# Performance work log

Measured on AMD Instinct MI355X. Metric: run time of the kernel, lower is better.

The kernel has to match this reference:

```python
import jax, jax.numpy as jnp
import numpy as np

N = 50000      # n_nodes
E = 800000     # n_edges (before self-loops)
IN = 256       # in_channels
MID = 512      # mid_channel
MID2 = MID // 2
OUT = 64       # out_channels


def setup_inputs() -> dict:
    key = jax.random.key(0)
    ks = jax.random.split(key, 16)
    def w(k, shape):
        fan_in = shape[0]
        return jax.random.normal(k, shape, jnp.float32) * (1.0 / np.sqrt(fan_in))
    return {
        "node_feature": jax.random.normal(ks[0], (N, IN), jnp.float32),
        "edge_index": jax.random.randint(ks[1], (2, E), 0, N, jnp.int32),
        # GCNConv weights (PyG convention: x @ W, bias added after aggregation)
        "Wg1": w(ks[2], (IN, MID)),   "bg1": jnp.zeros((MID,), jnp.float32),
        "Wg2": w(ks[3], (MID, MID2)), "bg2": jnp.zeros((MID2,), jnp.float32),
        "Wg3": w(ks[4], (MID2, OUT)), "bg3": jnp.zeros((OUT,), jnp.float32),
        # parallel Linear layers
        "Wl1": w(ks[5], (IN, MID)),   "bl1": jnp.zeros((MID,), jnp.float32),
        "Wl2": w(ks[6], (MID, MID2)), "bl2": jnp.zeros((MID2,), jnp.float32),
        "Wl3": w(ks[7], (MID2, OUT)), "bl3": jnp.zeros((OUT,), jnp.float32),
    }


def reference(node_feature, edge_index, Wg1, bg1, Wg2, bg2, Wg3, bg3,
              Wl1, bl1, Wl2, bl2, Wl3, bl3):
    n = node_feature.shape[0]
    # list_add_self_loops: append (i, i) for every node
    loops = jnp.arange(n, dtype=edge_index.dtype)
    src = jnp.concatenate([edge_index[0], loops])
    dst = jnp.concatenate([edge_index[1], loops])
    # symmetric GCN normalization: deg computed on graph with self-loops
    deg = jax.ops.segment_sum(jnp.ones_like(dst, jnp.float32), dst, num_segments=n)
    dis = jax.lax.rsqrt(jnp.maximum(deg, 1.0))  # deg >= 1 thanks to self-loops
    norm = dis[src] * dis[dst]                  # [E'] edge coefficients

    def gcn_conv(x, W, b):
        h = x @ W                                            # [N, F_out]
        msgs = h[src] * norm[:, None]                        # gather + scale
        return jax.ops.segment_sum(msgs, dst, num_segments=n) + b  # scatter-add

    h1 = jax.nn.elu(gcn_conv(node_feature, Wg1, bg1)) + node_feature @ Wl1 + bl1
    h2 = jax.nn.elu(gcn_conv(h1, Wg2, bg2)) + h1 @ Wl2 + bl2
    out = gcn_conv(h2, Wg3, bg3) + h2 @ Wl3 + bl3
    return out
```

## Files before the change

### kernel.cpp

```cpp
#include <hip/hip_runtime.h>
#include <hip/hip_bf16.h>
#include <math.h>

#define IN_CH  256
#define MID    512
#define MID2   256
#define OUT_CH 64

typedef __attribute__((ext_vector_type(8))) short s16x8;
typedef __attribute__((ext_vector_type(4))) float f32x4;


__global__ __launch_bounds__(256) void deg_kernel(const int* __restrict__ dst,
                                                  int* __restrict__ cnt, int E) {
  int stride = gridDim.x * blockDim.x;
  for (int e = blockIdx.x * blockDim.x + threadIdx.x; e < E; e += stride)
    atomicAdd(&cnt[dst[e]], 1);
}

__global__ __launch_bounds__(1024) void scan_dis_kernel(const int* __restrict__ cnt,
                                                        int* __restrict__ rowstart,
                                                        float* __restrict__ dis, int N) {
  __shared__ int part[1024];
  int t = threadIdx.x;
  int chunk = (N + 1023) >> 10;
  int lo = t * chunk;
  int hi = lo + chunk; if (hi > N) hi = N; if (lo > N) lo = N;
  int s = 0;
  for (int i = lo; i < hi; ++i) s += cnt[i] + 1;
  part[t] = s;
  __syncthreads();
  for (int off = 1; off < 1024; off <<= 1) {
    int v = (t >= off) ? part[t - off] : 0;
    __syncthreads();
    part[t] += v;
    __syncthreads();
  }
  int base = part[t] - s;
  for (int i = lo; i < hi; ++i) {
    int d = cnt[i] + 1;
    rowstart[i] = base;
    dis[i] = rsqrtf((float)d);
    base += d;
  }
  if (t == 1023) rowstart[N] = part[1023];
}

__global__ __launch_bounds__(256) void fill_adj_kernel(const int* __restrict__ src,
                                                       const int* __restrict__ dst,
                                                       const int* __restrict__ rowstart,
                                                       int* __restrict__ cnt2,
                                                       int* __restrict__ adj,
                                                       int E, int N) {
  int total = E + N;
  int stride = gridDim.x * blockDim.x;
  for (int e = blockIdx.x * blockDim.x + threadIdx.x; e < total; e += stride) {
    int s, d;
    if (e < E) { s = src[e]; d = dst[e]; }
    else       { s = d = e - E; }
    int pos = rowstart[d] + atomicAdd(&cnt2[d], 1);
    adj[pos] = s;
  }
}


__device__ inline unsigned bf16_rne(float v) {
  unsigned u = __float_as_uint(v);
  return (u + 0x7FFFu + ((u >> 16) & 1u)) >> 16;
}

__global__ __launch_bounds__(256) void wsplit_kernel(const float* __restrict__ W,
                                                     short* __restrict__ Wt_hi,
                                                     short* __restrict__ Wt_lo,
                                                     int K, int Fout) {
  int idx = blockIdx.x * 256 + threadIdx.x;
  if (idx >= K * Fout) return;
  int k = idx / Fout, n = idx - k * Fout;
  float v = W[idx];
  unsigned h = bf16_rne(v);
  float hf = __uint_as_float(h << 16);
  unsigned l = bf16_rne(v - hf);
  Wt_hi[(size_t)n * K + k] = (short)h;
  Wt_lo[(size_t)n * K + k] = (short)l;
}


template<bool ADD_BIAS>
__global__ __launch_bounds__(256, 2)
void gemm_mfma3(const float* __restrict__ A, const short* __restrict__ Bth,
                const short* __restrict__ Btl, const float* __restrict__ bias,
                float* __restrict__ C, int Nrows, int K, int Fout) {
  __shared__ short lds[4 * 128 * 64];
  short* Ah = lds;
  short* Al = lds + 8192;
  short* Bh = lds + 16384;
  short* Bl = lds + 24576;

  const int tid  = threadIdx.x;
  const int lane = tid & 63;
  const int wid  = tid >> 6;
  const int wr = wid >> 1, wc = wid & 1;
  const int row0 = blockIdx.x * 128;
  const int col0 = blockIdx.y * 128;

  f32x4 acc[4][4] = {};

  const int sr    = tid >> 1;
  const int shalf = (tid & 1) << 5;
  int arow = row0 + sr; if (arow > Nrows - 1) arow = Nrows - 1;
  const float* Abase  = A   + (size_t)arow * K + shalf;
  const short* Bhbase = Bth + (size_t)(col0 + sr) * K + shalf;
  const short* Blbase = Btl + (size_t)(col0 + sr) * K + shalf;
  int wslot[4];
  #pragma unroll
  for (int i = 0; i < 4; ++i)
    wslot[i] = sr * 64 + ((((shalf >> 3) + i) ^ (sr & 7)) << 3);

  for (int k0 = 0; k0 < K; k0 += 64) {
    float4 av[8];
    const float* ap = Abase + k0;
    #pragma unroll
    for (int i = 0; i < 8; ++i) av[i] = *(const float4*)(ap + i * 4);
    s16x8 rbh[4], rbl[4];
    const short* bp = Bhbase + k0;
    const short* bq = Blbase + k0;
    #pragma unroll
    for (int i = 0; i < 4; ++i) rbh[i] = *(const s16x8*)(bp + i * 8);
    #pragma unroll
    for (int i = 0; i < 4; ++i) rbl[i] = *(const s16x8*)(bq + i * 8);

    __syncthreads();

    #pragma unroll
    for (int i = 0; i < 4; ++i) {
      s16x8 hi, lo;
      #pragma unroll
      for (int j = 0; j < 2; ++j) {
        float4 v = av[i * 2 + j];
        float vv[4] = {v.x, v.y, v.z, v.w};
        #pragma unroll
        for (int m = 0; m < 4; ++m) {
          unsigned h = bf16_rne(vv[m]);
          float hf = __uint_as_float(h << 16);
          unsigned l = bf16_rne(vv[m] - hf);
          hi[j * 4 + m] = (short)h;
          lo[j * 4 + m] = (short)l;
        }
      }
      *(s16x8*)(Ah + wslot[i]) = hi;
      *(s16x8*)(Al + wslot[i]) = lo;
    }
    #pragma unroll
    for (int i = 0; i < 4; ++i) {
      *(s16x8*)(Bh + wslot[i]) = rbh[i];
      *(s16x8*)(Bl + wslot[i]) = rbl[i];
    }
    __syncthreads();

    #pragma unroll
    for (int ks = 0; ks < 2; ++ks) {
      const int sw = ((((ks << 2) + (lane >> 4)) ^ (lane & 7)) << 3);
      s16x8 fah[4], fal[4], fbh[4], fbl[4];
      #pragma unroll
      for (int mi = 0; mi < 4; ++mi) {
        int base = (wr * 64 + mi * 16 + (lane & 15)) * 64 + sw;
        fah[mi] = *(const s16x8*)(Ah + base);
        fal[mi] = *(const s16x8*)(Al + base);
      }
      #pragma unroll
      for (int ni = 0; ni < 4; ++ni) {
        int base = (wc * 64 + ni * 16 + (lane & 15)) * 64 + sw;
        fbh[ni] = *(const s16x8*)(Bh + base);
        fbl[ni] = *(const s16x8*)(Bl + base);
      }
      #pragma unroll
      for (int mi = 0; mi < 4; ++mi)
        #pragma unroll
        for (int ni = 0; ni < 4; ++ni) {
          acc[mi][ni] = __builtin_amdgcn_mfma_f32_16x16x32_bf16(fah[mi], fbh[ni], acc[mi][ni], 0, 0, 0);
          acc[mi][ni] = __builtin_amdgcn_mfma_f32_16x16x32_bf16(fah[mi], fbl[ni], acc[mi][ni], 0, 0, 0);
          acc[mi][ni] = __builtin_amdgcn_mfma_f32_16x16x32_bf16(fal[mi], fbh[ni], acc[mi][ni], 0, 0, 0);
        }
    }
  }

  #pragma unroll
  for (int mi = 0; mi < 4; ++mi) {
    #pragma unroll
    for (int r = 0; r < 4; ++r) {
      int rr = row0 + wr * 64 + mi * 16 + (lane >> 4) * 4 + r;
      if (rr >= Nrows) continue;
      #pragma unroll
      for (int ni = 0; ni < 4; ++ni) {
        int cc = col0 + wc * 64 + ni * 16 + (lane & 15);
        float v = acc[mi][ni][r];
        if (ADD_BIAS) v += bias[cc];
        C[(size_t)rr * Fout + cc] = v;
      }
    }
  }
}


template<bool ADD_BIAS>
__global__ __launch_bounds__(256) void gemm64(const float* __restrict__ A,
                                              const float* __restrict__ W,
                                              const float* __restrict__ bias,
                                              float* __restrict__ C,
                                              int Nrows, int K, int Fout) {
  __shared__ float As[16][64];
  __shared__ float Bs[16][64];
  const int tid  = threadIdx.x;
  const int row0 = blockIdx.x * 64;
  const int col0 = blockIdx.y * 64;
  const int tx   = tid & 15;
  const int ty   = tid >> 4;
  const int la_r = tid >> 2;
  const int la_c = (tid & 3) << 2;
  const int lb_r = tid >> 4;
  const int lb_c = (tid & 15) << 2;

  float acc[4][4];
  #pragma unroll
  for (int i = 0; i < 4; ++i)
    #pragma unroll
    for (int j = 0; j < 4; ++j) acc[i][j] = 0.f;

  for (int k0 = 0; k0 < K; k0 += 16) {
    float4 av = make_float4(0.f, 0.f, 0.f, 0.f);
    int ar = row0 + la_r;
    if (ar < Nrows) av = *(const float4*)(A + (size_t)ar * K + (k0 + la_c));
    float4 bv = *(const float4*)(W + (size_t)(k0 + lb_r) * Fout + (col0 + lb_c));
    __syncthreads();
    As[la_c + 0][la_r] = av.x;
    As[la_c + 1][la_r] = av.y;
    As[la_c + 2][la_r] = av.z;
    As[la_c + 3][la_r] = av.w;
    *(float4*)&Bs[lb_r][lb_c] = bv;
    __syncthreads();
    #pragma unroll
    for (int k = 0; k < 16; ++k) {
      float4 a4 = *(const float4*)&As[k][ty << 2];
      float4 b4 = *(const float4*)&Bs[k][tx << 2];
      float a[4] = {a4.x, a4.y, a4.z, a4.w};
      float b[4] = {b4.x, b4.y, b4.z, b4.w};
      #pragma unroll
      for (int i = 0; i < 4; ++i)
        #pragma unroll
        for (int j = 0; j < 4; ++j) acc[i][j] = fmaf(a[i], b[j], acc[i][j]);
    }
  }

  #pragma unroll
  for (int i = 0; i < 4; ++i) {
    int r = row0 + (ty << 2) + i;
    if (r < Nrows) {
      float4 v = make_float4(acc[i][0], acc[i][1], acc[i][2], acc[i][3]);
      if (ADD_BIAS) {
        const float* bp = bias + col0 + (tx << 2);
        v.x += bp[0]; v.y += bp[1]; v.z += bp[2]; v.w += bp[3];
      }
      *(float4*)(C + (size_t)r * Fout + col0 + (tx << 2)) = v;
    }
  }
}


__device__ inline void fma4(float4& a, const float4 q, const float w) {
  a.x = fmaf(q.x, w, a.x); a.y = fmaf(q.y, w, a.y);
  a.z = fmaf(q.z, w, a.z); a.w = fmaf(q.w, w, a.w);
}

template<int F, bool DO_ELU>
__global__ __launch_bounds__(256) void agg_kernel(const float* __restrict__ H,
                                                  const int* __restrict__ adj,
                                                  const int* __restrict__ rowstart,
                                                  const float* __restrict__ dis,
                                                  const float* __restrict__ bias,
                                                  float* __restrict__ out, int N) {
  constexpr int VF = F / 64;
  constexpr int NV = (VF >= 4) ? VF / 4 : 1;
  int node = (int)((blockIdx.x * blockDim.x + threadIdx.x) >> 6);
  int lane = threadIdx.x & 63;
  if (node >= N) return;
  int e = rowstart[node];
  const int end = rowstart[node + 1];

  if constexpr (VF >= 4) {
    float4 acc[NV] = {};
    const char* base = (const char*)H + (size_t)lane * (VF * 4);
    const size_t rstride = (size_t)F * 4;
    for (; e + 4 <= end; e += 4) {
      int s0 = adj[e], s1 = adj[e + 1], s2 = adj[e + 2], s3 = adj[e + 3];
      float w0 = dis[s0], w1 = dis[s1], w2 = dis[s2], w3 = dis[s3];
      const float4* p0 = (const float4*)(base + s0 * rstride);
      const float4* p1 = (const float4*)(base + s1 * rstride);
      const float4* p2 = (const float4*)(base + s2 * rstride);
      const float4* p3 = (const float4*)(base + s3 * rstride);
      #pragma unroll
      for (int v = 0; v < NV; ++v) {
        float4 q0 = p0[v], q1 = p1[v], q2 = p2[v], q3 = p3[v];
        fma4(acc[v], q0, w0); fma4(acc[v], q1, w1);
        fma4(acc[v], q2, w2); fma4(acc[v], q3, w3);
      }
    }
    for (; e < end; ++e) {
      int s = adj[e]; float w = dis[s];
      const float4* p = (const float4*)(base + s * rstride);
      #pragma unroll
      for (int v = 0; v < NV; ++v) fma4(acc[v], p[v], w);
    }
    float di = dis[node];
    float* op = out + (size_t)node * F + lane * VF;
    const float* bp = bias + lane * VF;
    #pragma unroll
    for (int v = 0; v < NV; ++v) {
      float vals[4] = {acc[v].x, acc[v].y, acc[v].z, acc[v].w};
      #pragma unroll
      for (int j = 0; j < 4; ++j) {
        float val = fmaf(vals[j], di, bp[v * 4 + j]);
        if (DO_ELU) val = (val > 0.f) ? val : expm1f(val);
        op[v * 4 + j] += val;
      }
    }
  } else {
    float acc = 0.f;
    for (; e + 4 <= end; e += 4) {
      int s0 = adj[e], s1 = adj[e + 1], s2 = adj[e + 2], s3 = adj[e + 3];
      float w0 = dis[s0], w1 = dis[s1], w2 = dis[s2], w3 = dis[s3];
      float q0 = H[(size_t)s0 * F + lane], q1 = H[(size_t)s1 * F + lane];
      float q2 = H[(size_t)s2 * F + lane], q3 = H[(size_t)s3 * F + lane];
      acc = fmaf(q0, w0, acc); acc = fmaf(q1, w1, acc);
      acc = fmaf(q2, w2, acc); acc = fmaf(q3, w3, acc);
    }
    for (; e < end; ++e) {
      int s = adj[e];
      acc = fmaf(H[(size_t)s * F + lane], dis[s], acc);
    }
    float val = fmaf(acc, dis[node], bias[lane]);
    if (DO_ELU) val = (val > 0.f) ? val : expm1f(val);
    out[(size_t)node * F + lane] += val;
  }
}


static inline char* ws_align(char*& ws, size_t bytes) {
  ws = (char*)(((uintptr_t)ws + 63) & ~(uintptr_t)63);
  char* p = ws;
  ws += bytes;
  return p;
}

extern "C" void kernel_launch(void* const* d_in, const int* in_sizes, int n_in,
                              void* d_out, int out_size, void* d_ws, size_t ws_size,
                              hipStream_t stream) {
  const float* x   = (const float*)d_in[0];
  const int*  eidx = (const int*)d_in[1];
  const float* Wg1 = (const float*)d_in[2];
  const float* bg1 = (const float*)d_in[3];
  const float* Wg2 = (const float*)d_in[4];
  const float* bg2 = (const float*)d_in[5];
  const float* Wg3 = (const float*)d_in[6];
  const float* bg3 = (const float*)d_in[7];
  const float* Wl1 = (const float*)d_in[8];
  const float* bl1 = (const float*)d_in[9];
  const float* Wl2 = (const float*)d_in[10];
  const float* bl2 = (const float*)d_in[11];
  const float* Wl3 = (const float*)d_in[12];
  const float* bl3 = (const float*)d_in[13];

  const int N = in_sizes[0] / IN_CH;
  const int E = in_sizes[1] / 2;
  const int* esrc = eidx;
  const int* edst = eidx + E;

  char* ws = (char*)d_ws;
  float* h1       = (float*)ws_align(ws, (size_t)N * MID  * 4);
  float* h2       = (float*)ws_align(ws, (size_t)N * MID2 * 4);
  float* Hb       = (float*)ws_align(ws, (size_t)N * MID  * 4);
  float* dis      = (float*)ws_align(ws, (size_t)N * 4);
  int*   rowstart = (int*)ws_align(ws, (size_t)(N + 1) * 4);
  int*   cnt      = (int*)ws_align(ws, (size_t)N * 4);
  int*   cnt2     = (int*)ws_align(ws, (size_t)N * 4);
  int*   adj      = (int*)ws_align(ws, (size_t)(E + N) * 4);
  short* wl1h = (short*)ws_align(ws, (size_t)IN_CH * MID  * 2);
  short* wl1l = (short*)ws_align(ws, (size_t)IN_CH * MID  * 2);
  short* wg1h = (short*)ws_align(ws, (size_t)IN_CH * MID  * 2);
  short* wg1l = (short*)ws_align(ws, (size_t)IN_CH * MID  * 2);
  short* wl2h = (short*)ws_align(ws, (size_t)MID * MID2 * 2);
  short* wl2l = (short*)ws_align(ws, (size_t)MID * MID2 * 2);
  short* wg2h = (short*)ws_align(ws, (size_t)MID * MID2 * 2);
  short* wg2l = (short*)ws_align(ws, (size_t)MID * MID2 * 2);

  hipMemsetAsync(cnt, 0, (size_t)2 * N * 4, stream);
  hipMemsetAsync(cnt2, 0, (size_t)N * 4, stream);
  deg_kernel<<<1024, 256, 0, stream>>>(edst, cnt, E);
  scan_dis_kernel<<<1, 1024, 0, stream>>>(cnt, rowstart, dis, N);
  fill_adj_kernel<<<2048, 256, 0, stream>>>(esrc, edst, rowstart, cnt2, adj, E, N);

  {
    int n1 = IN_CH * MID, n2 = MID * MID2;
    wsplit_kernel<<<(n1 + 255) / 256, 256, 0, stream>>>(Wl1, wl1h, wl1l, IN_CH, MID);
    wsplit_kernel<<<(n1 + 255) / 256, 256, 0, stream>>>(Wg1, wg1h, wg1l, IN_CH, MID);
    wsplit_kernel<<<(n2 + 255) / 256, 256, 0, stream>>>(Wl2, wl2h, wl2l, MID, MID2);
    wsplit_kernel<<<(n2 + 255) / 256, 256, 0, stream>>>(Wg2, wg2h, wg2l, MID, MID2);
  }

  int aggBlocks = (N + 3) / 4;
  int rowBlocks = (N + 127) / 128;

  dim3 g1(rowBlocks, MID / 128);
  gemm_mfma3<true ><<<g1, 256, 0, stream>>>(x, wl1h, wl1l, bl1, h1, N, IN_CH, MID);
  gemm_mfma3<false><<<g1, 256, 0, stream>>>(x, wg1h, wg1l, nullptr, Hb, N, IN_CH, MID);
  agg_kernel<MID, true><<<aggBlocks, 256, 0, stream>>>(Hb, adj, rowstart, dis, bg1, h1, N);

  dim3 g2(rowBlocks, MID2 / 128);
  gemm_mfma3<true ><<<g2, 256, 0, stream>>>(h1, wl2h, wl2l, bl2, h2, N, MID, MID2);
  gemm_mfma3<false><<<g2, 256, 0, stream>>>(h1, wg2h, wg2l, nullptr, Hb, N, MID, MID2);
  agg_kernel<MID2, true><<<aggBlocks, 256, 0, stream>>>(Hb, adj, rowstart, dis, bg2, h2, N);

  float* outp = (float*)d_out;
  dim3 g3((N + 63) / 64, OUT_CH / 64);
  gemm64<true ><<<g3, 256, 0, stream>>>(h2, Wl3, bl3, outp, N, MID2, OUT_CH);
  gemm64<false><<<g3, 256, 0, stream>>>(h2, Wg3, nullptr, Hb, N, MID2, OUT_CH);
  agg_kernel<OUT_CH, false><<<aggBlocks, 256, 0, stream>>>(Hb, adj, rowstart, dis, bg3, outp, N);
}
```

Before: 1.062 ms.

## Fuse linear and GCN GEMMs per layer, store GCN features in bf16

```diff
diff --git a/kernel.cpp b/kernel.cpp
--- a/kernel.cpp
+++ b/kernel.cpp
@@ -69,27 +69,28 @@
   return (u + 0x7FFFu + ((u >> 16) & 1u)) >> 16;
 }
 
-__global__ __launch_bounds__(256) void wsplit_kernel(const float* __restrict__ W,
-                                                     short* __restrict__ Wt_hi,
-                                                     short* __restrict__ Wt_lo,
-                                                     int K, int Fout) {
+__global__ __launch_bounds__(256) void wsplit_cat(const float* __restrict__ W,
+                                                  short* __restrict__ Th,
+                                                  short* __restrict__ Tl,
+                                                  int K, int F, int noff) {
   int idx = blockIdx.x * 256 + threadIdx.x;
-  if (idx >= K * Fout) return;
-  int k = idx / Fout, n = idx - k * Fout;
+  if (idx >= K * F) return;
+  int k = idx / F, n = idx - k * F;
   float v = W[idx];
   unsigned h = bf16_rne(v);
   float hf = __uint_as_float(h << 16);
   unsigned l = bf16_rne(v - hf);
-  Wt_hi[(size_t)n * K + k] = (short)h;
-  Wt_lo[(size_t)n * K + k] = (short)l;
-}
-
-
-template<bool ADD_BIAS>
+  Th[(size_t)(noff + n) * K + k] = (short)h;
+  Tl[(size_t)(noff + n) * K + k] = (short)l;
+}
+
+
+template<bool OUT2_BF16>
 __global__ __launch_bounds__(256, 2)
-void gemm_mfma3(const float* __restrict__ A, const short* __restrict__ Bth,
-                const short* __restrict__ Btl, const float* __restrict__ bias,
-                float* __restrict__ C, int Nrows, int K, int Fout) {
+void gemm_dual(const float* __restrict__ A, const short* __restrict__ Bth,
+               const short* __restrict__ Btl, const float* __restrict__ bias1,
+               float* __restrict__ C1, void* __restrict__ C2,
+               int Nrows, int K, int F1) {
   __shared__ short lds[4 * 128 * 64];
   short* Ah = lds;
   short* Al = lds + 8192;
@@ -194,153 +195,101 @@
       for (int ni = 0; ni < 4; ++ni) {
         int cc = col0 + wc * 64 + ni * 16 + (lane & 15);
         float v = acc[mi][ni][r];
-        if (ADD_BIAS) v += bias[cc];
-        C[(size_t)rr * Fout + cc] = v;
+        if (cc < F1) {
+          C1[(size_t)rr * F1 + cc] = v + bias1[cc];
+        } else {
+          int c2 = cc - F1;
+          if (OUT2_BF16)
+            ((unsigned short*)C2)[(size_t)rr * F1 + c2] = (unsigned short)bf16_rne(v);
+          else
+            ((float*)C2)[(size_t)rr * F1 + c2] = v;
+        }
       }
     }
   }
 }
 
 
-template<bool ADD_BIAS>
-__global__ __launch_bounds__(256) void gemm64(const float* __restrict__ A,
-                                              const float* __restrict__ W,
-                                              const float* __restrict__ bias,
-                                              float* __restrict__ C,
-                                              int Nrows, int K, int Fout) {
-  __shared__ float As[16][64];
-  __shared__ float Bs[16][64];
-  const int tid  = threadIdx.x;
-  const int row0 = blockIdx.x * 64;
-  const int col0 = blockIdx.y * 64;
-  const int tx   = tid & 15;
-  const int ty   = tid >> 4;
-  const int la_r = tid >> 2;
-  const int la_c = (tid & 3) << 2;
-  const int lb_r = tid >> 4;
-  const int lb_c = (tid & 15) << 2;
-
-  float acc[4][4];
-  #pragma unroll
-  for (int i = 0; i < 4; ++i)
-    #pragma unroll
-    for (int j = 0; j < 4; ++j) acc[i][j] = 0.f;
-
-  for (int k0 = 0; k0 < K; k0 += 16) {
-    float4 av = make_float4(0.f, 0.f, 0.f, 0.f);
-    int ar = row0 + la_r;
-    if (ar < Nrows) av = *(const float4*)(A + (size_t)ar * K + (k0 + la_c));
-    float4 bv = *(const float4*)(W + (size_t)(k0 + lb_r) * Fout + (col0 + lb_c));
-    __syncthreads();
-    As[la_c + 0][la_r] = av.x;
-    As[la_c + 1][la_r] = av.y;
-    As[la_c + 2][la_r] = av.z;
-    As[la_c + 3][la_r] = av.w;
-    *(float4*)&Bs[lb_r][lb_c] = bv;
-    __syncthreads();
-    #pragma unroll
-    for (int k = 0; k < 16; ++k) {
-      float4 a4 = *(const float4*)&As[k][ty << 2];
-      float4 b4 = *(const float4*)&Bs[k][tx << 2];
-      float a[4] = {a4.x, a4.y, a4.z, a4.w};
-      float b[4] = {b4.x, b4.y, b4.z, b4.w};
-      #pragma unroll
-      for (int i = 0; i < 4; ++i)
-        #pragma unroll
-        for (int j = 0; j < 4; ++j) acc[i][j] = fmaf(a[i], b[j], acc[i][j]);
-    }
-  }
-
-  #pragma unroll
-  for (int i = 0; i < 4; ++i) {
-    int r = row0 + (ty << 2) + i;
-    if (r < Nrows) {
-      float4 v = make_float4(acc[i][0], acc[i][1], acc[i][2], acc[i][3]);
-      if (ADD_BIAS) {
-        const float* bp = bias + col0 + (tx << 2);
-        v.x += bp[0]; v.y += bp[1]; v.z += bp[2]; v.w += bp[3];
-      }
-      *(float4*)(C + (size_t)r * Fout + col0 + (tx << 2)) = v;
-    }
-  }
-}
-
-
-__device__ inline void fma4(float4& a, const float4 q, const float w) {
-  a.x = fmaf(q.x, w, a.x); a.y = fmaf(q.y, w, a.y);
-  a.z = fmaf(q.z, w, a.z); a.w = fmaf(q.w, w, a.w);
-}
-
 template<int F, bool DO_ELU>
-__global__ __launch_bounds__(256) void agg_kernel(const float* __restrict__ H,
-                                                  const int* __restrict__ adj,
-                                                  const int* __restrict__ rowstart,
-                                                  const float* __restrict__ dis,
-                                                  const float* __restrict__ bias,
-                                                  float* __restrict__ out, int N) {
+__global__ __launch_bounds__(256) void agg_bf16(const unsigned short* __restrict__ H,
+                                                const int* __restrict__ adj,
+                                                const int* __restrict__ rowstart,
+                                                const float* __restrict__ dis,
+                                                const float* __restrict__ bias,
+                                                float* __restrict__ out, int N) {
   constexpr int VF = F / 64;
-  constexpr int NV = (VF >= 4) ? VF / 4 : 1;
+  typedef __attribute__((ext_vector_type(VF))) unsigned short uvec;
   int node = (int)((blockIdx.x * blockDim.x + threadIdx.x) >> 6);
   int lane = threadIdx.x & 63;
   if (node >= N) return;
   int e = rowstart[node];
   const int end = rowstart[node + 1];
 
-  if constexpr (VF >= 4) {
-    float4 acc[NV] = {};
-    const char* base = (const char*)H + (size_t)lane * (VF * 4);
-    const size_t rstride = (size_t)F * 4;
-    for (; e + 4 <= end; e += 4) {
-      int s0 = adj[e], s1 = adj[e + 1], s2 = adj[e + 2], s3 = adj[e + 3];
-      float w0 = dis[s0], w1 = dis[s1], w2 = dis[s2], w3 = dis[s3];
-      const float4* p0 = (const float4*)(base + s0 * rstride);
-      const float4* p1 = (const float4*)(base + s1 * rstride);
-      const float4* p2 = (const float4*)(base + s2 * rstride);
-      const float4* p3 = (const float4*)(base + s3 * rstride);
-      #pragma unroll
-      for (int v = 0; v < NV; ++v) {
-        float4 q0 = p0[v], q1 = p1[v], q2 = p2[v], q3 = p3[v];
-        fma4(acc[v], q0, w0); fma4(acc[v], q1, w1);
-        fma4(acc[v], q2, w2); fma4(acc[v], q3, w3);
-      }
-    }
-    for (; e < end; ++e) {
-      int s = adj[e]; float w = dis[s];
-      const float4* p = (const float4*)(base + s * rstride);
-      #pragma unroll
-      for (int v = 0; v < NV; ++v) fma4(acc[v], p[v], w);
-    }
-    float di = dis[node];
-    float* op = out + (size_t)node * F + lane * VF;
-    const float* bp = bias + lane * VF;
-    #pragma unroll
-    for (int v = 0; v < NV; ++v) {
-      float vals[4] = {acc[v].x, acc[v].y, acc[v].z, acc[v].w};
-      #pragma unroll
-      for (int j = 0; j < 4; ++j) {
-        float val = fmaf(vals[j], di, bp[v * 4 + j]);
-        if (DO_ELU) val = (val > 0.f) ? val : expm1f(val);
-        op[v * 4 + j] += val;
-      }
-    }
-  } else {
-    float acc = 0.f;
-    for (; e + 4 <= end; e += 4) {
-      int s0 = adj[e], s1 = adj[e + 1], s2 = adj[e + 2], s3 = adj[e + 3];
-      float w0 = dis[s0], w1 = dis[s1], w2 = dis[s2], w3 = dis[s3];
-      float q0 = H[(size_t)s0 * F + lane], q1 = H[(size_t)s1 * F + lane];
-      float q2 = H[(size_t)s2 * F + lane], q3 = H[(size_t)s3 * F + lane];
-      acc = fmaf(q0, w0, acc); acc = fmaf(q1, w1, acc);
-      acc = fmaf(q2, w2, acc); acc = fmaf(q3, w3, acc);
-    }
-    for (; e < end; ++e) {
-      int s = adj[e];
-      acc = fmaf(H[(size_t)s * F + lane], dis[s], acc);
-    }
-    float val = fmaf(acc, dis[node], bias[lane]);
+  float acc[VF] = {};
+  const unsigned short* base = H + (size_t)lane * VF;
+  for (; e + 4 <= end; e += 4) {
+    int s0 = adj[e], s1 = adj[e + 1], s2 = adj[e + 2], s3 = adj[e + 3];
+    float w0 = dis[s0], w1 = dis[s1], w2 = dis[s2], w3 = dis[s3];
+    uvec v0 = *(const uvec*)(base + (size_t)s0 * F);
+    uvec v1 = *(const uvec*)(base + (size_t)s1 * F);
+    uvec v2 = *(const uvec*)(base + (size_t)s2 * F);
+    uvec v3 = *(const uvec*)(base + (size_t)s3 * F);
+    #pragma unroll
+    for (int j = 0; j < VF; ++j) {
+      acc[j] = fmaf(__uint_as_float((unsigned)v0[j] << 16), w0, acc[j]);
+      acc[j] = fmaf(__uint_as_float((unsigned)v1[j] << 16), w1, acc[j]);
+      acc[j] = fmaf(__uint_as_float((unsigned)v2[j] << 16), w2, acc[j]);
+      acc[j] = fmaf(__uint_as_float((unsigned)v3[j] << 16), w3, acc[j]);
+    }
+  }
+  for (; e < end; ++e) {
+    int s = adj[e]; float w = dis[s];
+    uvec v = *(const uvec*)(base + (size_t)s * F);
+    #pragma unroll
+    for (int j = 0; j < VF; ++j)
+      acc[j] = fmaf(__uint_as_float((unsigned)v[j] << 16), w, acc[j]);
+  }
+
+  float di = dis[node];
+  float* op = out + (size_t)node * F + lane * VF;
+  const float* bp = bias + lane * VF;
+  #pragma unroll
+  for (int j = 0; j < VF; ++j) {
+    float val = fmaf(acc[j], di, bp[j]);
     if (DO_ELU) val = (val > 0.f) ? val : expm1f(val);
-    out[(size_t)node * F + lane] += val;
-  }
+    op[j] += val;
+  }
+}
+
+
+template<int F, bool DO_ELU>
+__global__ __launch_bounds__(256) void agg_f32(const float* __restrict__ H,
+                                               const int* __restrict__ adj,
+                                               const int* __restrict__ rowstart,
+                                               const float* __restrict__ dis,
+                                               const float* __restrict__ bias,
+                                               float* __restrict__ out, int N) {
+  int node = (int)((blockIdx.x * blockDim.x + threadIdx.x) >> 6);
+  int lane = threadIdx.x & 63;
+  if (node >= N) return;
+  int e = rowstart[node];
+  const int end = rowstart[node + 1];
+  float acc = 0.f;
+  for (; e + 4 <= end; e += 4) {
+    int s0 = adj[e], s1 = adj[e + 1], s2 = adj[e + 2], s3 = adj[e + 3];
+    float w0 = dis[s0], w1 = dis[s1], w2 = dis[s2], w3 = dis[s3];
+    float q0 = H[(size_t)s0 * F + lane], q1 = H[(size_t)s1 * F + lane];
+    float q2 = H[(size_t)s2 * F + lane], q3 = H[(size_t)s3 * F + lane];
+    acc = fmaf(q0, w0, acc); acc = fmaf(q1, w1, acc);
+    acc = fmaf(q2, w2, acc); acc = fmaf(q3, w3, acc);
+  }
+  for (; e < end; ++e) {
+    int s = adj[e];
+    acc = fmaf(H[(size_t)s * F + lane], dis[s], acc);
+  }
+  float val = fmaf(acc, dis[node], bias[lane]);
+  if (DO_ELU) val = (val > 0.f) ? val : expm1f(val);
+  out[(size_t)node * F + lane] += val;
 }
 
 
@@ -375,53 +324,51 @@
   const int* edst = eidx + E;
 
   char* ws = (char*)d_ws;
-  float* h1       = (float*)ws_align(ws, (size_t)N * MID  * 4);
-  float* h2       = (float*)ws_align(ws, (size_t)N * MID2 * 4);
-  float* Hb       = (float*)ws_align(ws, (size_t)N * MID  * 4);
+  float* h1   = (float*)ws_align(ws, (size_t)N * MID  * 4);
+  float* h2   = (float*)ws_align(ws, (size_t)N * MID2 * 4);
+  unsigned short* Hbf = (unsigned short*)ws_align(ws, (size_t)N * MID * 2);
+  float* Hb3  = (float*)ws_align(ws, (size_t)N * OUT_CH * 4);
   float* dis      = (float*)ws_align(ws, (size_t)N * 4);
   int*   rowstart = (int*)ws_align(ws, (size_t)(N + 1) * 4);
   int*   cnt      = (int*)ws_align(ws, (size_t)N * 4);
   int*   cnt2     = (int*)ws_align(ws, (size_t)N * 4);
   int*   adj      = (int*)ws_align(ws, (size_t)(E + N) * 4);
-  short* wl1h = (short*)ws_align(ws, (size_t)IN_CH * MID  * 2);
-  short* wl1l = (short*)ws_align(ws, (size_t)IN_CH * MID  * 2);
-  short* wg1h = (short*)ws_align(ws, (size_t)IN_CH * MID  * 2);
-  short* wg1l = (short*)ws_align(ws, (size_t)IN_CH * MID  * 2);
-  short* wl2h = (short*)ws_align(ws, (size_t)MID * MID2 * 2);
-  short* wl2l = (short*)ws_align(ws, (size_t)MID * MID2 * 2);
-  short* wg2h = (short*)ws_align(ws, (size_t)MID * MID2 * 2);
-  short* wg2l = (short*)ws_align(ws, (size_t)MID * MID2 * 2);
-
-  hipMemsetAsync(cnt, 0, (size_t)2 * N * 4, stream);
+  short* w1h = (short*)ws_align(ws, (size_t)1024 * IN_CH * 2);
+  short* w1l = (short*)ws_align(ws, (size_t)1024 * IN_CH * 2);
+  short* w2h = (short*)ws_align(ws, (size_t)512 * MID * 2);
+  short* w2l = (short*)ws_align(ws, (size_t)512 * MID * 2);
+  short* w3h = (short*)ws_align(ws, (size_t)128 * MID2 * 2);
+  short* w3l = (short*)ws_align(ws, (size_t)128 * MID2 * 2);
+
+  hipMemsetAsync(cnt, 0, (size_t)N * 4, stream);
   hipMemsetAsync(cnt2, 0, (size_t)N * 4, stream);
   deg_kernel<<<1024, 256, 0, stream>>>(edst, cnt, E);
   scan_dis_kernel<<<1, 1024, 0, stream>>>(cnt, rowstart, dis, N);
   fill_adj_kernel<<<2048, 256, 0, stream>>>(esrc, edst, rowstart, cnt2, adj, E, N);
 
   {
-    int n1 = IN_CH * MID, n2 = MID * MID2;
-    wsplit_kernel<<<(n1 + 255) / 256, 256, 0, stream>>>(Wl1, wl1h, wl1l, IN_CH, MID);
-    wsplit_kernel<<<(n1 + 255) / 256, 256, 0, stream>>>(Wg1, wg1h, wg1l, IN_CH, MID);
-    wsplit_kernel<<<(n2 + 255) / 256, 256, 0, stream>>>(Wl2, wl2h, wl2l, MID, MID2);
-    wsplit_kernel<<<(n2 + 255) / 256, 256, 0, stream>>>(Wg2, wg2h, wg2l, MID, MID2);
-  }
-
-  int aggBlocks = (N + 3) / 4;
-  int rowBlocks = (N + 127) / 128;
-
-  dim3 g1(rowBlocks, MID / 128);
-  gemm_mfma3<true ><<<g1, 256, 0, stream>>>(x, wl1h, wl1l, bl1, h1, N, IN_CH, MID);
-  gemm_mfma3<false><<<g1, 256, 0, stream>>>(x, wg1h, wg1l, nullptr, Hb, N, IN_CH, MID);
-  agg_kernel<MID, true><<<aggBlocks, 256, 0, stream>>>(Hb, adj, rowstart, dis, bg1, h1, N);
-
-  dim3 g2(rowBlocks, MID2 / 128);
-  gemm_mfma3<true ><<<g2, 256, 0, stream>>>(h1, wl2h, wl2l, bl2, h2, N, MID, MID2);
-  gemm_mfma3<false><<<g2, 256, 0, stream>>>(h1, wg2h, wg2l, nullptr, Hb, N, MID, MID2);
-  agg_kernel<MID2, true><<<aggBlocks, 256, 0, stream>>>(Hb, adj, rowstart, dis, bg2, h2, N);
+    int n1 = IN_CH * MID, n2 = MID * MID2, n3 = MID2 * OUT_CH;
+    wsplit_cat<<<(n1 + 255) / 256, 256, 0, stream>>>(Wl1, w1h, w1l, IN_CH, MID, 0);
+    wsplit_cat<<<(n1 + 255) / 256, 256, 0, stream>>>(Wg1, w1h, w1l, IN_CH, MID, MID);
+    wsplit_cat<<<(n2 + 255) / 256, 256, 0, stream>>>(Wl2, w2h, w2l, MID, MID2, 0);
+    wsplit_cat<<<(n2 + 255) / 256, 256, 0, stream>>>(Wg2, w2h, w2l, MID, MID2, MID2);
+    wsplit_cat<<<(n3 + 255) / 256, 256, 0, stream>>>(Wl3, w3h, w3l, MID2, OUT_CH, 0);
+    wsplit_cat<<<(n3 + 255) / 256, 256, 0, stream>>>(Wg3, w3h, w3l, MID2, OUT_CH, OUT_CH);
+  }
+
+  const int aggBlocks = (N + 3) / 4;
+  const int rowBlocks = (N + 127) / 128;
+
+  dim3 g1(rowBlocks, (2 * MID) / 128);
+  gemm_dual<true><<<g1, 256, 0, stream>>>(x, w1h, w1l, bl1, h1, Hbf, N, IN_CH, MID);
+  agg_bf16<MID, true><<<aggBlocks, 256, 0, stream>>>(Hbf, adj, rowstart, dis, bg1, h1, N);
+
+  dim3 g2(rowBlocks, (2 * MID2) / 128);
+  gemm_dual<true><<<g2, 256, 0, stream>>>(h1, w2h, w2l, bl2, h2, Hbf, N, MID, MID2);
+  agg_bf16<MID2, true><<<aggBlocks, 256, 0, stream>>>(Hbf, adj, rowstart, dis, bg2, h2, N);
 
   float* outp = (float*)d_out;
-  dim3 g3((N + 63) / 64, OUT_CH / 64);
-  gemm64<true ><<<g3, 256, 0, stream>>>(h2, Wl3, bl3, outp, N, MID2, OUT_CH);
-  gemm64<false><<<g3, 256, 0, stream>>>(h2, Wg3, nullptr, Hb, N, MID2, OUT_CH);
-  agg_kernel<OUT_CH, false><<<aggBlocks, 256, 0, stream>>>(Hb, adj, rowstart, dis, bg3, outp, N);
-}
+  dim3 g3(rowBlocks, (2 * OUT_CH) / 128);
+  gemm_dual<false><<<g3, 256, 0, stream>>>(h2, w3h, w3l, bl3, outp, Hb3, N, MID2, OUT_CH);
+  agg_f32<OUT_CH, false><<<aggBlocks, 256, 0, stream>>>(Hb3, adj, rowstart, dis, bg3, outp, N);
+}
```

Result: faster. 894.0 us (-15.8%).
